# Kernel optimization log

Measured on AMD Instinct MI355X. Metric: run time of the kernel, lower is better.

The kernel has to match this reference:

```python
import jax, jax.numpy as jnp
import numpy as np

C_IN, C_OUT, K, H = 64, 128, 27, 100000

def setup_inputs() -> dict:
    key = jax.random.key(0)
    k1, k2, k3 = jax.random.split(key, 3)
    data_in = jax.random.normal(k1, (1, C_IN, H, 1), dtype=jnp.float32)
    # neighbor index table: 27 neighbors per node; -1 would mean 'missing' (zero-padded)
    neigh = jax.random.randint(k2, (H, K), 0, H, dtype=jnp.int64)
    # conv weight, fan-in scaled init, stored [C_out, C_in, K]
    weight = jax.random.normal(k3, (C_OUT, C_IN, K), dtype=jnp.float32) / np.sqrt(C_IN * K)
    return {"data_in": data_in, "neigh": neigh, "weight": weight}

def reference(data_in, neigh, weight):
    # data_in: [1, C_in, H, 1] (ocnn layout) -> [C_in, H]
    x = data_in[0, :, :, 0]
    # octree2col: gather 27 neighbors per node -> [C_in, H, K]
    cols = x[:, neigh]
    # zero out missing neighbors (index < 0)
    cols = jnp.where(neigh[None, :, :] >= 0, cols, jnp.zeros((), dtype=cols.dtype))
    # GEMM over (C_in, K) fused with ReLU -> [C_out, H]
    out = jnp.einsum('chk,ock->oh', cols, weight)
    out = jax.nn.relu(out)
    return out[None, :, :, None]  # back to ocnn layout [1, C_out, H, 1]
```

## Files before the change

kernel.cpp:

```cpp
#include <hip/hip_runtime.h>
#include <hip/hip_bf16.h>

#define C_IN  64
#define C_OUT 128
#define KK    27
#define HH    100000
#define TB    1563
#define WB    108
#define NBLK  782

typedef __attribute__((ext_vector_type(8))) short s8v;
typedef __attribute__((ext_vector_type(4))) float f32x4;

__device__ inline unsigned short f2bf(float f) {
    __hip_bfloat16 h = __float2bfloat16(f);
    return *reinterpret_cast<unsigned short*>(&h);
}

__device__ inline void dma16(const void* g, void* l) {
    __builtin_amdgcn_global_load_lds((const __attribute__((address_space(1))) void*)g,
                                     (__attribute__((address_space(3))) void*)l, 16, 0, 0);
}

__global__ __launch_bounds__(256) void prep_kernel(const float* __restrict__ x,
                                                   const float* __restrict__ w,
                                                   unsigned short* __restrict__ xt,
                                                   unsigned short* __restrict__ wk) {
    const int tid = threadIdx.x;
    if (blockIdx.x < TB) {
        __shared__ __align__(16) unsigned short ts[64 * 72];
        const int hbase = blockIdx.x * 64;
        #pragma unroll
        for (int it = 0; it < 16; ++it) {
            int i = it * 256 + tid;
            int c = i >> 6, hl = i & 63;
            int hg = hbase + hl;
            float v = (hg < HH) ? x[(size_t)c * HH + hg] : 0.f;
            ts[hl * 72 + c] = f2bf(v);
        }
        __syncthreads();
        #pragma unroll
        for (int it = 0; it < 2; ++it) {
            int u = it * 256 + tid;
            int hl = u >> 3, part = u & 7;
            int hg = hbase + hl;
            if (hg < HH)
                *(int4*)&xt[(size_t)hg * 64 + part * 8] = *(const int4*)&ts[hl * 72 + part * 8];
        }
    } else {
        int b = blockIdx.x - TB;
        int base = b * 2048 + tid;
        #pragma unroll
        for (int j = 0; j < 8; ++j) {
            int t = base + j * 256;
            int jj = t & 63, o = (t >> 6) & 127, kx = t >> 13;
            int lc = (jj >> 3) ^ (o & 7);
            int c  = lc * 8 + (jj & 7);
            wk[t] = f2bf(w[(size_t)o * (C_IN * KK) + c * KK + kx]);
        }
    }
}

__global__ __launch_bounds__(256, 3) void conv_main(const unsigned short* __restrict__ xt,
                                                    const unsigned short* __restrict__ wk,
                                                    const int* __restrict__ neigh,
                                                    float* __restrict__ out) {
    __shared__ int neigh_s[128 * KK];
    __shared__ __align__(16) unsigned short w_s[2][128 * 64];

    const int tid  = threadIdx.x;
    const int wave = tid >> 6;
    const int lane = tid & 63;
    const int col  = lane & 15;
    const int quad = lane >> 4;
    const int hbase = blockIdx.x * 128;

    for (int i = tid; i < 128 * KK; i += 256) {
        int hl = i / KK, kx = i - hl * KK;
        int hg = hbase + hl;
        neigh_s[i] = (hg < HH) ? neigh[(size_t)hg * KK + kx] : -1;
    }

    auto dmaW = [&](int k, int b) {
        const unsigned short* src = wk + (size_t)k * (C_OUT * C_IN);
        #pragma unroll
        for (int i = 0; i < 4; ++i) {
            int row_base = wave * 8 + i * 32;
            dma16(src + row_base * 64 + lane * 8, &w_s[b][row_base * 64]);
        }
    };

    dmaW(0, 0);

    f32x4 acc[8][2];
    #pragma unroll
    for (int mt = 0; mt < 8; ++mt) {
        acc[mt][0] = (f32x4){0.f, 0.f, 0.f, 0.f};
        acc[mt][1] = (f32x4){0.f, 0.f, 0.f, 0.f};
    }

    __syncthreads();

    const int pc_b = quad * 8;
    auto loadB = [&](int kk, int4 (&B)[4]) {
        #pragma unroll
        for (int nt = 0; nt < 2; ++nt) {
            int n = wave * 32 + nt * 16 + col;
            int idx = neigh_s[n * KK + kk];
            if (idx >= 0) {
                const unsigned short* base = xt + (size_t)idx * 64 + pc_b;
                B[nt]     = *(const int4*)(base);
                B[2 + nt] = *(const int4*)(base + 32);
            } else {
                B[nt]     = make_int4(0, 0, 0, 0);
                B[2 + nt] = make_int4(0, 0, 0, 0);
            }
        }
    };

    auto mfma_phase = [&](const unsigned short* wbuf, int4 (&B)[4]) {
        #pragma unroll
        for (int ch = 0; ch < 2; ++ch) {
            const int pc = (ch * 4 + quad) ^ (col & 7);
            #pragma unroll
            for (int mt = 0; mt < 8; ++mt) {
                s8v a = *(const s8v*)&wbuf[(mt * 16 + col) * 64 + pc * 8];
                acc[mt][0] = __builtin_amdgcn_mfma_f32_16x16x32_bf16(a, __builtin_bit_cast(s8v, B[ch * 2 + 0]), acc[mt][0], 0, 0, 0);
                acc[mt][1] = __builtin_amdgcn_mfma_f32_16x16x32_bf16(a, __builtin_bit_cast(s8v, B[ch * 2 + 1]), acc[mt][1], 0, 0, 0);
            }
        }
    };

    int4 B0[4], B1[4];
    loadB(0, B0);

    #pragma unroll 1
    for (int kb = 0; kb < 13; ++kb) {
        int k = kb * 2;
        dmaW(k + 1, 1);
        loadB(k + 1, B1);
        mfma_phase(w_s[0], B0);
        __syncthreads();

        if (k + 2 < KK) {
            dmaW(k + 2, 0);
            loadB(k + 2, B0);
        }
        mfma_phase(w_s[1], B1);
        __syncthreads();
    }
    mfma_phase(w_s[0], B0);

    #pragma unroll
    for (int mt = 0; mt < 8; ++mt) {
        #pragma unroll
        for (int nt = 0; nt < 2; ++nt) {
            int hg = hbase + wave * 32 + nt * 16 + col;
            if (hg < HH) {
                #pragma unroll
                for (int r = 0; r < 4; ++r) {
                    int o = mt * 16 + quad * 4 + r;
                    float v = acc[mt][nt][r];
                    out[(size_t)o * HH + hg] = v > 0.f ? v : 0.f;
                }
            }
        }
    }
}

extern "C" void kernel_launch(void* const* d_in, const int* in_sizes, int n_in,
                              void* d_out, int out_size, void* d_ws, size_t ws_size,
                              hipStream_t stream) {
    const float* data_in = (const float*)d_in[0];
    const int*   neigh   = (const int*)d_in[1];
    const float* weight  = (const float*)d_in[2];
    float* out = (float*)d_out;

    unsigned short* xt = (unsigned short*)d_ws;
    unsigned short* wk = xt + (size_t)HH * 64;

    prep_kernel<<<TB + WB, 256, 0, stream>>>(data_in, weight, xt, wk);
    conv_main<<<NBLK, 256, 0, stream>>>(xt, wk, neigh, out);
}
```

Baseline: 186.8 us.

## Read conv weights directly from global and drop LDS staging and barriers

Removes the double-buffered LDS weight staging (async global-to-LDS DMA plus two block barriers per step). Each wave now loads its A fragments straight from the global weight buffer, relying on L1/L2 caching, so the XOR swizzle in the weight prep is dropped. Blocks shrink to 2 waves covering 96 nodes, and each wave handles 3 N-tiles instead of 2, so every weight fragment feeds more MFMAs. The trade-off is that weight-load latency is no longer hidden behind an explicit prefetch and more global and L1 traffic is generated per MFMA.

Measured after the change: 315.1 us. 68.7% more time.

```diff
diff --git a/kernel.cpp b/kernel.cpp
--- a/kernel.cpp
+++ b/kernel.cpp
@@ -7,7 +7,8 @@
 #define HH    100000
 #define TB    1563
 #define WB    108
-#define NBLK  782
+#define BH    96
+#define NBLK  1042
 
 typedef __attribute__((ext_vector_type(8))) short s8v;
 typedef __attribute__((ext_vector_type(4))) float f32x4;
@@ -15,11 +16,6 @@
 __device__ inline unsigned short f2bf(float f) {
     __hip_bfloat16 h = __float2bfloat16(f);
     return *reinterpret_cast<unsigned short*>(&h);
-}
-
-__device__ inline void dma16(const void* g, void* l) {
-    __builtin_amdgcn_global_load_lds((const __attribute__((address_space(1))) void*)g,
-                                     (__attribute__((address_space(3))) void*)l, 16, 0, 0);
 }
 
 __global__ __launch_bounds__(256) void prep_kernel(const float* __restrict__ x,
@@ -53,109 +49,93 @@
         #pragma unroll
         for (int j = 0; j < 8; ++j) {
             int t = base + j * 256;
-            int jj = t & 63, o = (t >> 6) & 127, kx = t >> 13;
-            int lc = (jj >> 3) ^ (o & 7);
-            int c  = lc * 8 + (jj & 7);
+            int c = t & 63, o = (t >> 6) & 127, kx = t >> 13;
             wk[t] = f2bf(w[(size_t)o * (C_IN * KK) + c * KK + kx]);
         }
     }
 }
 
-__global__ __launch_bounds__(256, 3) void conv_main(const unsigned short* __restrict__ xt,
+__global__ __launch_bounds__(128, 2) void conv_main(const unsigned short* __restrict__ xt,
                                                     const unsigned short* __restrict__ wk,
                                                     const int* __restrict__ neigh,
                                                     float* __restrict__ out) {
-    __shared__ int neigh_s[128 * KK];
-    __shared__ __align__(16) unsigned short w_s[2][128 * 64];
+    __shared__ int neigh_s[BH * KK];
 
     const int tid  = threadIdx.x;
     const int wave = tid >> 6;
     const int lane = tid & 63;
     const int col  = lane & 15;
     const int quad = lane >> 4;
-    const int hbase = blockIdx.x * 128;
+    const int hbase = blockIdx.x * BH;
 
-    for (int i = tid; i < 128 * KK; i += 256) {
+    for (int i = tid; i < BH * KK; i += 128) {
         int hl = i / KK, kx = i - hl * KK;
         int hg = hbase + hl;
         neigh_s[i] = (hg < HH) ? neigh[(size_t)hg * KK + kx] : -1;
     }
 
-    auto dmaW = [&](int k, int b) {
-        const unsigned short* src = wk + (size_t)k * (C_OUT * C_IN);
+    f32x4 acc[8][3];
+    #pragma unroll
+    for (int mt = 0; mt < 8; ++mt)
         #pragma unroll
-        for (int i = 0; i < 4; ++i) {
-            int row_base = wave * 8 + i * 32;
-            dma16(src + row_base * 64 + lane * 8, &w_s[b][row_base * 64]);
-        }
-    };
-
-    dmaW(0, 0);
-
-    f32x4 acc[8][2];
-    #pragma unroll
-    for (int mt = 0; mt < 8; ++mt) {
-        acc[mt][0] = (f32x4){0.f, 0.f, 0.f, 0.f};
-        acc[mt][1] = (f32x4){0.f, 0.f, 0.f, 0.f};
-    }
+        for (int nt = 0; nt < 3; ++nt)
+            acc[mt][nt] = (f32x4){0.f, 0.f, 0.f, 0.f};
 
     __syncthreads();
 
-    const int pc_b = quad * 8;
-    auto loadB = [&](int kk, int4 (&B)[4]) {
+    const unsigned short* xq = xt + quad * 8;
+
+    auto loadB = [&](int kk, int4 (&B)[2][3]) {
         #pragma unroll
-        for (int nt = 0; nt < 2; ++nt) {
-            int n = wave * 32 + nt * 16 + col;
+        for (int nt = 0; nt < 3; ++nt) {
+            int n = wave * 48 + nt * 16 + col;
             int idx = neigh_s[n * KK + kk];
             if (idx >= 0) {
-                const unsigned short* base = xt + (size_t)idx * 64 + pc_b;
-                B[nt]     = *(const int4*)(base);
-                B[2 + nt] = *(const int4*)(base + 32);
+                const unsigned short* base = xq + (size_t)idx * 64;
+                B[0][nt] = *(const int4*)(base);
+                B[1][nt] = *(const int4*)(base + 32);
             } else {
-                B[nt]     = make_int4(0, 0, 0, 0);
-                B[2 + nt] = make_int4(0, 0, 0, 0);
+                B[0][nt] = make_int4(0, 0, 0, 0);
+                B[1][nt] = make_int4(0, 0, 0, 0);
             }
         }
     };
 
-    auto mfma_phase = [&](const unsigned short* wbuf, int4 (&B)[4]) {
+    const unsigned short* wbase = wk + col * 64 + quad * 8;
+
+    auto mfmaK = [&](int k, int4 (&B)[2][3]) {
+        const unsigned short* wp = wbase + (size_t)k * (C_OUT * C_IN);
         #pragma unroll
         for (int ch = 0; ch < 2; ++ch) {
-            const int pc = (ch * 4 + quad) ^ (col & 7);
             #pragma unroll
             for (int mt = 0; mt < 8; ++mt) {
-                s8v a = *(const s8v*)&wbuf[(mt * 16 + col) * 64 + pc * 8];
-                acc[mt][0] = __builtin_amdgcn_mfma_f32_16x16x32_bf16(a, __builtin_bit_cast(s8v, B[ch * 2 + 0]), acc[mt][0], 0, 0, 0);
-                acc[mt][1] = __builtin_amdgcn_mfma_f32_16x16x32_bf16(a, __builtin_bit_cast(s8v, B[ch * 2 + 1]), acc[mt][1], 0, 0, 0);
+                s8v a = *(const s8v*)(wp + mt * 1024 + ch * 32);
+                #pragma unroll
+                for (int nt = 0; nt < 3; ++nt)
+                    acc[mt][nt] = __builtin_amdgcn_mfma_f32_16x16x32_bf16(
+                        a, __builtin_bit_cast(s8v, B[ch][nt]), acc[mt][nt], 0, 0, 0);
             }
         }
     };
 
-    int4 B0[4], B1[4];
+    int4 B0[2][3], B1[2][3];
     loadB(0, B0);
 
     #pragma unroll 1
     for (int kb = 0; kb < 13; ++kb) {
         int k = kb * 2;
-        dmaW(k + 1, 1);
         loadB(k + 1, B1);
-        mfma_phase(w_s[0], B0);
-        __syncthreads();
-
-        if (k + 2 < KK) {
-            dmaW(k + 2, 0);
-            loadB(k + 2, B0);
-        }
-        mfma_phase(w_s[1], B1);
-        __syncthreads();
+        mfmaK(k, B0);
+        loadB(k + 2, B0);
+        mfmaK(k + 1, B1);
     }
-    mfma_phase(w_s[0], B0);
+    mfmaK(26, B0);
 
     #pragma unroll
     for (int mt = 0; mt < 8; ++mt) {
         #pragma unroll
-        for (int nt = 0; nt < 2; ++nt) {
-            int hg = hbase + wave * 32 + nt * 16 + col;
+        for (int nt = 0; nt < 3; ++nt) {
+            int hg = hbase + wave * 48 + nt * 16 + col;
             if (hg < HH) {
                 #pragma unroll
                 for (int r = 0; r < 4; ++r) {
@@ -180,5 +160,5 @@
     unsigned short* wk = xt + (size_t)HH * 64;
 
     prep_kernel<<<TB + WB, 256, 0, stream>>>(data_in, weight, xt, wk);
-    conv_main<<<NBLK, 256, 0, stream>>>(xt, wk, neigh, out);
+    conv_main<<<NBLK, 128, 0, stream>>>(xt, wk, neigh, out);
 }
```
